# Kernel tuning notes

Hardware: AMD Instinct MI355X
Metric: run time of the kernel (lower is better)

Reference implementation:

```python
import jax, jax.numpy as jnp
import numpy as np

N_POINTS = 100000
N_EVENTS = 1000000
N_PAIRS = 100000      # node_pair_samples
N_RIEMANN = 128       # riemann_samples
INIT_BETA = 0.025
NON_EVENT_W = 1.0
EPS = 1e-6            # torch PairwiseDistance default eps (added to the difference)


def setup_inputs() -> dict:
    key = jax.random.key(0)
    ks = jax.random.split(key, 8)
    # learned parameters
    beta = jnp.full((1, 1), INIT_BETA, jnp.float32)
    z0 = jax.random.uniform(ks[0], (N_POINTS, 2), jnp.float32, -0.025, 0.025)
    v0 = jax.random.uniform(ks[1], (N_POINTS, 2), jnp.float32, -0.025, 0.025)
    a0 = jnp.zeros((N_POINTS, 2), jnp.float32)  # a0 is referenced by step(); zero -> constant-velocity
    # event data: (u, v, event_time)
    u = jax.random.randint(ks[2], (N_EVENTS,), 0, N_POINTS)
    v = jax.random.randint(ks[3], (N_EVENTS,), 0, N_POINTS)
    event_times = jax.random.uniform(ks[4], (N_EVENTS,), jnp.float32, 0.0, 1.0)
    # sampled non-event node pairs (stand-in for randperm over triu indices)
    pair_u = jax.random.randint(ks[5], (N_PAIRS,), 0, N_POINTS)
    pair_v = jax.random.randint(ks[6], (N_PAIRS,), 0, N_POINTS)
    pair_v = jnp.where(pair_v == pair_u, (pair_v + 1) % N_POINTS, pair_v)
    t0 = jnp.float32(0.0)
    tn = jnp.float32(1.0)
    return {"beta": beta, "z0": z0, "v0": v0, "a0": a0,
            "u": u, "v": v, "event_times": event_times,
            "pair_u": pair_u, "pair_v": pair_v, "t0": t0, "tn": tn}


def reference(beta, z0, v0, a0, u, v, event_times, pair_u, pair_v, t0, tn):
    b = beta[0, 0]
    # ---- event intensity: sum_e (beta - ||z_u(t_e) - z_v(t_e)||) ----
    te = event_times[:, None]                                  # [E,1]
    zu = z0[u] + v0[u] * te + 0.5 * a0[u] * te ** 2            # [E,2]
    zv = z0[v] + v0[v] * te + 0.5 * a0[v] * te ** 2            # [E,2]
    d_ev = jnp.sqrt(jnp.sum((zu - zv + EPS) ** 2, axis=-1))    # [E]
    event_intensity = b * event_times.shape[0] - jnp.sum(d_ev)
    # ---- non-event intensity: Riemann sum of exp(beta - d(t)) over sampled pairs ----
    ts = t0 + (jnp.arange(N_RIEMANN, dtype=jnp.float32) / N_RIEMANN) * (tn - t0)  # [T] left Riemann
    dt = (tn - t0) / N_RIEMANN
    dz = z0[pair_u] - z0[pair_v]                               # [P,2]
    dv = v0[pair_u] - v0[pair_v]
    da = a0[pair_u] - a0[pair_v]
    tt = ts[None, :, None]                                     # [1,T,1]
    diff = dz[:, None, :] + dv[:, None, :] * tt + 0.5 * da[:, None, :] * tt ** 2 + EPS  # [P,T,2]
    d_ne = jnp.sqrt(jnp.sum(diff ** 2, axis=-1))               # [P,T]
    non_event_intensity = jnp.sum(jnp.exp(b - d_ne)) * dt
    return event_intensity - NON_EVENT_W * non_event_intensity
```

## Files before the change

### kernel.cpp

```cpp
#include <hip/hip_runtime.h>
#include <hip/hip_fp16.h>

#define N_POINTS   100000
#define N_EVENTS   1000000
#define N_PAIRS    100000
#define N_RIEMANN  128
#define EPS_F      1e-6f
#define NON_EVENT_W 1.0f

constexpr int BLOCK       = 256;

constexpr int EVPT        = 8;
constexpr int EV_THREADS  = N_EVENTS / EVPT;
constexpr int EV_BLOCKS   = (EV_THREADS + BLOCK - 1) / BLOCK;

constexpr int RPT          = 32;
constexpr int CHUNKS       = N_RIEMANN / RPT;
constexpr int PAIR_THREADS = N_PAIRS * CHUNKS;
constexpr int PAIR_BLOCKS  = (PAIR_THREADS + BLOCK - 1) / BLOCK;

constexpr int MAIN_BLOCKS = PAIR_BLOCKS + EV_BLOCKS;
constexpr int PREP_BLOCKS = (N_POINTS + BLOCK - 1) / BLOCK;


__device__ __forceinline__ float block_reduce_sum(float v) {
    #pragma unroll
    for (int off = 32; off > 0; off >>= 1)
        v += __shfl_down(v, off, 64);
    __shared__ float smem[BLOCK / 64];
    const int lane = threadIdx.x & 63;
    const int wid  = threadIdx.x >> 6;
    if (lane == 0) smem[wid] = v;
    __syncthreads();
    float r = 0.f;
    if (threadIdx.x == 0) {
        #pragma unroll
        for (int i = 0; i < BLOCK / 64; ++i) r += smem[i];
    }
    return r;
}

__device__ __forceinline__ void decode_rec(const float4& r, float2& z, float2& v, float2& a) {
    z = __half22float2(*reinterpret_cast<const __half2*>(&r.x));
    v = __half22float2(*reinterpret_cast<const __half2*>(&r.y));
    a = __half22float2(*reinterpret_cast<const __half2*>(&r.z));
}

__global__ __launch_bounds__(BLOCK) void prep_kernel(
    const float2* __restrict__ z0,
    const float2* __restrict__ v0,
    const float2* __restrict__ a0,
    float4*       __restrict__ pts)
{
    const int i = blockIdx.x * BLOCK + threadIdx.x;
    if (i < N_POINTS) {
        const float2 z = z0[i], v = v0[i], a = a0[i];
        float4 r;
        *reinterpret_cast<__half2*>(&r.x) = __float22half2_rn(make_float2(z.x, z.y));
        *reinterpret_cast<__half2*>(&r.y) = __float22half2_rn(make_float2(v.x, v.y));
        *reinterpret_cast<__half2*>(&r.z) = __float22half2_rn(make_float2(a.x, a.y));
        r.w = 0.f;
        pts[i] = r;
    }
}

template <bool PACKED>
__global__ __launch_bounds__(BLOCK) void main_kernel(
    const float4* __restrict__ pts,
    const float2* __restrict__ z0,
    const float2* __restrict__ v0,
    const float2* __restrict__ a0,
    const float*  __restrict__ beta,
    const int*    __restrict__ eu,
    const int*    __restrict__ ev,
    const float*  __restrict__ et,
    const int*    __restrict__ pu,
    const int*    __restrict__ pv,
    const float*  __restrict__ t0p,
    const float*  __restrict__ tnp,
    float*        __restrict__ partials)
{
    float acc = 0.f;
    const int b = blockIdx.x;

    if (b < PAIR_BLOCKS) {
        const int p = b * BLOCK + threadIdx.x;
        if (p < PAIR_THREADS) {
            const int chunk = p / N_PAIRS;
            const int pr    = p - chunk * N_PAIRS;
            const float t0v = t0p[0];
            const float tnv = tnp[0];
            const float step = (tnv - t0v) * (1.0f / N_RIEMANN);
            const float bb  = beta[0];
            const int iu = pu[pr];
            const int iv = pv[pr];
            float dzx, dzy, dvx, dvy, dax, day;
            if (PACKED) {
                const float4 ru = pts[iu];
                const float4 rv = pts[iv];
                float2 zu, vu, au, zv, vv, av;
                decode_rec(ru, zu, vu, au);
                decode_rec(rv, zv, vv, av);
                dzx = zu.x - zv.x; dzy = zu.y - zv.y;
                dvx = vu.x - vv.x; dvy = vu.y - vv.y;
                dax = au.x - av.x; day = au.y - av.y;
            } else {
                const float2 zu = z0[iu], zv = z0[iv];
                const float2 vu = v0[iu], vv = v0[iv];
                const float2 au = a0[iu], av = a0[iv];
                dzx = zu.x - zv.x; dzy = zu.y - zv.y;
                dvx = vu.x - vv.x; dvy = vu.y - vv.y;
                dax = au.x - av.x; day = au.y - av.y;
            }
            const float dzxe = dzx + EPS_F;
            const float dzye = dzy + EPS_F;
            const float hax  = 0.5f * dax;
            const float hay  = 0.5f * day;
            const float eb = __expf(bb);
            float s = 0.f;
            const int k0 = chunk * RPT;
            #pragma unroll 8
            for (int k = k0; k < k0 + RPT; ++k) {
                const float t  = __fmaf_rn((float)k, step, t0v);
                const float h  = t * t;
                const float dx = __fmaf_rn(hax, h, __fmaf_rn(dvx, t, dzxe));
                const float dy = __fmaf_rn(hay, h, __fmaf_rn(dvy, t, dzye));
                const float d  = __builtin_amdgcn_sqrtf(__fmaf_rn(dy, dy, dx * dx));
                s += __expf(-d);
            }
            acc = -NON_EVENT_W * step * eb * s;
        }
    } else {
        const int t = (b - PAIR_BLOCKS) * BLOCK + threadIdx.x;
        if (t < EV_THREADS) {
            const int4*   eu4 = reinterpret_cast<const int4*>(eu);
            const int4*   ev4 = reinterpret_cast<const int4*>(ev);
            const float4* et4 = reinterpret_cast<const float4*>(et);
            const int4 u0 = eu4[2 * t], u1 = eu4[2 * t + 1];
            const int4 w0 = ev4[2 * t], w1 = ev4[2 * t + 1];
            const float4 t0q = et4[2 * t], t1q = et4[2 * t + 1];
            const int iu[EVPT] = { u0.x, u0.y, u0.z, u0.w, u1.x, u1.y, u1.z, u1.w };
            const int iv[EVPT] = { w0.x, w0.y, w0.z, w0.w, w1.x, w1.y, w1.z, w1.w };
            const float te[EVPT] = { t0q.x, t0q.y, t0q.z, t0q.w, t1q.x, t1q.y, t1q.z, t1q.w };
            if (PACKED) {
                float4 ru[EVPT], rv[EVPT];
                #pragma unroll
                for (int j = 0; j < EVPT; ++j) ru[j] = pts[iu[j]];
                #pragma unroll
                for (int j = 0; j < EVPT; ++j) rv[j] = pts[iv[j]];
                #pragma unroll
                for (int j = 0; j < EVPT; ++j) {
                    float2 zu, vu, au, zv, vv, av;
                    decode_rec(ru[j], zu, vu, au);
                    decode_rec(rv[j], zv, vv, av);
                    const float h = 0.5f * te[j] * te[j];
                    const float dx = (zu.x - zv.x) + (vu.x - vv.x) * te[j] + (au.x - av.x) * h + EPS_F;
                    const float dy = (zu.y - zv.y) + (vu.y - vv.y) * te[j] + (au.y - av.y) * h + EPS_F;
                    acc -= __builtin_amdgcn_sqrtf(__fmaf_rn(dy, dy, dx * dx));
                }
            } else {
                #pragma unroll
                for (int j = 0; j < EVPT; ++j) {
                    const float2 zu = z0[iu[j]], zv = z0[iv[j]];
                    const float2 vu = v0[iu[j]], vv = v0[iv[j]];
                    const float2 au = a0[iu[j]], av = a0[iv[j]];
                    const float h = 0.5f * te[j] * te[j];
                    const float dx = (zu.x - zv.x) + (vu.x - vv.x) * te[j] + (au.x - av.x) * h + EPS_F;
                    const float dy = (zu.y - zv.y) + (vu.y - vv.y) * te[j] + (au.y - av.y) * h + EPS_F;
                    acc -= __builtin_amdgcn_sqrtf(__fmaf_rn(dy, dy, dx * dx));
                }
            }
        }
    }

    const float r = block_reduce_sum(acc);
    if (threadIdx.x == 0) partials[blockIdx.x] = r;
}

__global__ __launch_bounds__(BLOCK) void reduce_kernel(
    const float* __restrict__ partials,
    const float* __restrict__ beta,
    float*       __restrict__ out)
{
    float acc = 0.f;
    for (int i = threadIdx.x; i < MAIN_BLOCKS; i += BLOCK) acc += partials[i];
    const float r = block_reduce_sum(acc);
    if (threadIdx.x == 0) out[0] = beta[0] * (float)N_EVENTS + r;
}

extern "C" void kernel_launch(void* const* d_in, const int* in_sizes, int n_in,
                              void* d_out, int out_size, void* d_ws, size_t ws_size,
                              hipStream_t stream) {
    const float*  beta = (const float*)d_in[0];
    const float2* z0   = (const float2*)d_in[1];
    const float2* v0   = (const float2*)d_in[2];
    const float2* a0   = (const float2*)d_in[3];
    const int*    eu   = (const int*)d_in[4];
    const int*    ev   = (const int*)d_in[5];
    const float*  et   = (const float*)d_in[6];
    const int*    pu   = (const int*)d_in[7];
    const int*    pv   = (const int*)d_in[8];
    const float*  t0p  = (const float*)d_in[9];
    const float*  tnp  = (const float*)d_in[10];

    float* out = (float*)d_out;
    const size_t pts_bytes = (size_t)N_POINTS * sizeof(float4);
    const bool packed = (ws_size >= pts_bytes + (size_t)MAIN_BLOCKS * sizeof(float));

    if (packed) {
        float4* pts      = (float4*)d_ws;
        float*  partials = (float*)((char*)d_ws + pts_bytes);
        prep_kernel<<<PREP_BLOCKS, BLOCK, 0, stream>>>(z0, v0, a0, pts);
        main_kernel<true><<<MAIN_BLOCKS, BLOCK, 0, stream>>>(
            pts, z0, v0, a0, beta, eu, ev, et, pu, pv, t0p, tnp, partials);
        reduce_kernel<<<1, BLOCK, 0, stream>>>(partials, beta, out);
    } else {
        float* partials = (float*)d_ws;
        main_kernel<false><<<MAIN_BLOCKS, BLOCK, 0, stream>>>(
            nullptr, z0, v0, a0, beta, eu, ev, et, pu, pv, t0p, tnp, partials);
        reduce_kernel<<<1, BLOCK, 0, stream>>>(partials, beta, out);
    }
}
```

Measured before the change: 101.8 us.

## Fuse prep, main and reduce kernels into one cooperative persistent kernel

Replaces the three launches (fp16 packing, main compute, final reduce) with a single cooperative kernel that uses grid-wide syncs between phases. A persistent grid sized from occupancy for 256 CUs loops over the virtual blocks, with event blocks now ordered before pair blocks. This removes launch gaps and two kernel boundaries, but adds grid-sync overhead and cooperative-launch constraints. Block 0 does the final reduction after the second grid sync.

```diff
diff --git a/kernel.cpp b/kernel.cpp
--- a/kernel.cpp
+++ b/kernel.cpp
@@ -1,5 +1,8 @@
 #include <hip/hip_runtime.h>
 #include <hip/hip_fp16.h>
+#include <hip/hip_cooperative_groups.h>
+
+namespace cg = cooperative_groups;
 
 #define N_POINTS   100000
 #define N_EVENTS   1000000
@@ -8,19 +11,18 @@
 #define EPS_F      1e-6f
 #define NON_EVENT_W 1.0f
 
-constexpr int BLOCK       = 256;
-
-constexpr int EVPT        = 8;
-constexpr int EV_THREADS  = N_EVENTS / EVPT;
-constexpr int EV_BLOCKS   = (EV_THREADS + BLOCK - 1) / BLOCK;
+constexpr int BLOCK = 256;
+
+constexpr int EVPT       = 8;
+constexpr int EV_THREADS = N_EVENTS / EVPT;
+constexpr int EV_BLOCKS  = (EV_THREADS + BLOCK - 1) / BLOCK;
 
 constexpr int RPT          = 32;
 constexpr int CHUNKS       = N_RIEMANN / RPT;
 constexpr int PAIR_THREADS = N_PAIRS * CHUNKS;
 constexpr int PAIR_BLOCKS  = (PAIR_THREADS + BLOCK - 1) / BLOCK;
 
-constexpr int MAIN_BLOCKS = PAIR_BLOCKS + EV_BLOCKS;
-constexpr int PREP_BLOCKS = (N_POINTS + BLOCK - 1) / BLOCK;
+constexpr int VB_TOTAL = EV_BLOCKS + PAIR_BLOCKS;
 
 
 __device__ __forceinline__ float block_reduce_sum(float v) {
@@ -46,27 +48,9 @@
     a = __half22float2(*reinterpret_cast<const __half2*>(&r.z));
 }
 
-__global__ __launch_bounds__(BLOCK) void prep_kernel(
-    const float2* __restrict__ z0,
-    const float2* __restrict__ v0,
-    const float2* __restrict__ a0,
-    float4*       __restrict__ pts)
-{
-    const int i = blockIdx.x * BLOCK + threadIdx.x;
-    if (i < N_POINTS) {
-        const float2 z = z0[i], v = v0[i], a = a0[i];
-        float4 r;
-        *reinterpret_cast<__half2*>(&r.x) = __float22half2_rn(make_float2(z.x, z.y));
-        *reinterpret_cast<__half2*>(&r.y) = __float22half2_rn(make_float2(v.x, v.y));
-        *reinterpret_cast<__half2*>(&r.z) = __float22half2_rn(make_float2(a.x, a.y));
-        r.w = 0.f;
-        pts[i] = r;
-    }
-}
-
 template <bool PACKED>
-__global__ __launch_bounds__(BLOCK) void main_kernel(
-    const float4* __restrict__ pts,
+__global__ __launch_bounds__(BLOCK) void fused_kernel(
+    float4*       __restrict__ pts,
     const float2* __restrict__ z0,
     const float2* __restrict__ v0,
     const float2* __restrict__ a0,
@@ -78,114 +62,129 @@
     const int*    __restrict__ pv,
     const float*  __restrict__ t0p,
     const float*  __restrict__ tnp,
-    float*        __restrict__ partials)
+    float*        __restrict__ partials,
+    float*        __restrict__ out)
 {
+    const int G = gridDim.x;
+
+    if constexpr (PACKED) {
+        for (int i = blockIdx.x * BLOCK + threadIdx.x; i < N_POINTS; i += G * BLOCK) {
+            const float2 z = z0[i], v = v0[i], a = a0[i];
+            float4 r;
+            *reinterpret_cast<__half2*>(&r.x) = __float22half2_rn(make_float2(z.x, z.y));
+            *reinterpret_cast<__half2*>(&r.y) = __float22half2_rn(make_float2(v.x, v.y));
+            *reinterpret_cast<__half2*>(&r.z) = __float22half2_rn(make_float2(a.x, a.y));
+            r.w = 0.f;
+            pts[i] = r;
+        }
+        cg::this_grid().sync();
+    }
+
+    const float t0v  = t0p[0];
+    const float tnv  = tnp[0];
+    const float bb   = beta[0];
+    const float step = (tnv - t0v) * (1.0f / N_RIEMANN);
+    const float neg_dt_eb = -NON_EVENT_W * step * __expf(bb);
+
     float acc = 0.f;
-    const int b = blockIdx.x;
-
-    if (b < PAIR_BLOCKS) {
-        const int p = b * BLOCK + threadIdx.x;
-        if (p < PAIR_THREADS) {
-            const int chunk = p / N_PAIRS;
-            const int pr    = p - chunk * N_PAIRS;
-            const float t0v = t0p[0];
-            const float tnv = tnp[0];
-            const float step = (tnv - t0v) * (1.0f / N_RIEMANN);
-            const float bb  = beta[0];
-            const int iu = pu[pr];
-            const int iv = pv[pr];
-            float dzx, dzy, dvx, dvy, dax, day;
-            if (PACKED) {
-                const float4 ru = pts[iu];
-                const float4 rv = pts[iv];
-                float2 zu, vu, au, zv, vv, av;
-                decode_rec(ru, zu, vu, au);
-                decode_rec(rv, zv, vv, av);
-                dzx = zu.x - zv.x; dzy = zu.y - zv.y;
-                dvx = vu.x - vv.x; dvy = vu.y - vv.y;
-                dax = au.x - av.x; day = au.y - av.y;
-            } else {
-                const float2 zu = z0[iu], zv = z0[iv];
-                const float2 vu = v0[iu], vv = v0[iv];
-                const float2 au = a0[iu], av = a0[iv];
-                dzx = zu.x - zv.x; dzy = zu.y - zv.y;
-                dvx = vu.x - vv.x; dvy = vu.y - vv.y;
-                dax = au.x - av.x; day = au.y - av.y;
-            }
-            const float dzxe = dzx + EPS_F;
-            const float dzye = dzy + EPS_F;
-            const float hax  = 0.5f * dax;
-            const float hay  = 0.5f * day;
-            const float eb = __expf(bb);
-            float s = 0.f;
-            const int k0 = chunk * RPT;
-            #pragma unroll 8
-            for (int k = k0; k < k0 + RPT; ++k) {
-                const float t  = __fmaf_rn((float)k, step, t0v);
-                const float h  = t * t;
-                const float dx = __fmaf_rn(hax, h, __fmaf_rn(dvx, t, dzxe));
-                const float dy = __fmaf_rn(hay, h, __fmaf_rn(dvy, t, dzye));
-                const float d  = __builtin_amdgcn_sqrtf(__fmaf_rn(dy, dy, dx * dx));
-                s += __expf(-d);
-            }
-            acc = -NON_EVENT_W * step * eb * s;
-        }
-    } else {
-        const int t = (b - PAIR_BLOCKS) * BLOCK + threadIdx.x;
-        if (t < EV_THREADS) {
-            const int4*   eu4 = reinterpret_cast<const int4*>(eu);
-            const int4*   ev4 = reinterpret_cast<const int4*>(ev);
-            const float4* et4 = reinterpret_cast<const float4*>(et);
-            const int4 u0 = eu4[2 * t], u1 = eu4[2 * t + 1];
-            const int4 w0 = ev4[2 * t], w1 = ev4[2 * t + 1];
-            const float4 t0q = et4[2 * t], t1q = et4[2 * t + 1];
-            const int iu[EVPT] = { u0.x, u0.y, u0.z, u0.w, u1.x, u1.y, u1.z, u1.w };
-            const int iv[EVPT] = { w0.x, w0.y, w0.z, w0.w, w1.x, w1.y, w1.z, w1.w };
-            const float te[EVPT] = { t0q.x, t0q.y, t0q.z, t0q.w, t1q.x, t1q.y, t1q.z, t1q.w };
-            if (PACKED) {
-                float4 ru[EVPT], rv[EVPT];
-                #pragma unroll
-                for (int j = 0; j < EVPT; ++j) ru[j] = pts[iu[j]];
-                #pragma unroll
-                for (int j = 0; j < EVPT; ++j) rv[j] = pts[iv[j]];
-                #pragma unroll
-                for (int j = 0; j < EVPT; ++j) {
-                    float2 zu, vu, au, zv, vv, av;
-                    decode_rec(ru[j], zu, vu, au);
-                    decode_rec(rv[j], zv, vv, av);
-                    const float h = 0.5f * te[j] * te[j];
-                    const float dx = (zu.x - zv.x) + (vu.x - vv.x) * te[j] + (au.x - av.x) * h + EPS_F;
-                    const float dy = (zu.y - zv.y) + (vu.y - vv.y) * te[j] + (au.y - av.y) * h + EPS_F;
-                    acc -= __builtin_amdgcn_sqrtf(__fmaf_rn(dy, dy, dx * dx));
-                }
-            } else {
-                #pragma unroll
-                for (int j = 0; j < EVPT; ++j) {
-                    const float2 zu = z0[iu[j]], zv = z0[iv[j]];
-                    const float2 vu = v0[iu[j]], vv = v0[iv[j]];
-                    const float2 au = a0[iu[j]], av = a0[iv[j]];
-                    const float h = 0.5f * te[j] * te[j];
-                    const float dx = (zu.x - zv.x) + (vu.x - vv.x) * te[j] + (au.x - av.x) * h + EPS_F;
-                    const float dy = (zu.y - zv.y) + (vu.y - vv.y) * te[j] + (au.y - av.y) * h + EPS_F;
-                    acc -= __builtin_amdgcn_sqrtf(__fmaf_rn(dy, dy, dx * dx));
+
+    for (int vb = blockIdx.x; vb < VB_TOTAL; vb += G) {
+        if (vb < EV_BLOCKS) {
+            const int t = vb * BLOCK + threadIdx.x;
+            if (t < EV_THREADS) {
+                const int4*   eu4 = reinterpret_cast<const int4*>(eu);
+                const int4*   ev4 = reinterpret_cast<const int4*>(ev);
+                const float4* et4 = reinterpret_cast<const float4*>(et);
+                const int4 u0 = eu4[2 * t], u1 = eu4[2 * t + 1];
+                const int4 w0 = ev4[2 * t], w1 = ev4[2 * t + 1];
+                const float4 t0q = et4[2 * t], t1q = et4[2 * t + 1];
+                const int iu[EVPT] = { u0.x, u0.y, u0.z, u0.w, u1.x, u1.y, u1.z, u1.w };
+                const int iv[EVPT] = { w0.x, w0.y, w0.z, w0.w, w1.x, w1.y, w1.z, w1.w };
+                const float te[EVPT] = { t0q.x, t0q.y, t0q.z, t0q.w, t1q.x, t1q.y, t1q.z, t1q.w };
+                if constexpr (PACKED) {
+                    float4 ru[EVPT], rv[EVPT];
+                    #pragma unroll
+                    for (int j = 0; j < EVPT; ++j) ru[j] = pts[iu[j]];
+                    #pragma unroll
+                    for (int j = 0; j < EVPT; ++j) rv[j] = pts[iv[j]];
+                    #pragma unroll
+                    for (int j = 0; j < EVPT; ++j) {
+                        float2 zu, vu, au, zv, vv, av;
+                        decode_rec(ru[j], zu, vu, au);
+                        decode_rec(rv[j], zv, vv, av);
+                        const float h = 0.5f * te[j] * te[j];
+                        const float dx = (zu.x - zv.x) + (vu.x - vv.x) * te[j] + (au.x - av.x) * h + EPS_F;
+                        const float dy = (zu.y - zv.y) + (vu.y - vv.y) * te[j] + (au.y - av.y) * h + EPS_F;
+                        acc -= __builtin_amdgcn_sqrtf(__fmaf_rn(dy, dy, dx * dx));
+                    }
+                } else {
+                    #pragma unroll
+                    for (int j = 0; j < EVPT; ++j) {
+                        const float2 zu = z0[iu[j]], zv = z0[iv[j]];
+                        const float2 vu = v0[iu[j]], vv = v0[iv[j]];
+                        const float2 au = a0[iu[j]], av = a0[iv[j]];
+                        const float h = 0.5f * te[j] * te[j];
+                        const float dx = (zu.x - zv.x) + (vu.x - vv.x) * te[j] + (au.x - av.x) * h + EPS_F;
+                        const float dy = (zu.y - zv.y) + (vu.y - vv.y) * te[j] + (au.y - av.y) * h + EPS_F;
+                        acc -= __builtin_amdgcn_sqrtf(__fmaf_rn(dy, dy, dx * dx));
+                    }
                 }
             }
+        } else {
+            const int p = (vb - EV_BLOCKS) * BLOCK + threadIdx.x;
+            if (p < PAIR_THREADS) {
+                const int chunk = p / N_PAIRS;
+                const int pr    = p - chunk * N_PAIRS;
+                const int iu = pu[pr];
+                const int iv = pv[pr];
+                float dzx, dzy, dvx, dvy, dax, day;
+                if constexpr (PACKED) {
+                    const float4 ru = pts[iu];
+                    const float4 rv = pts[iv];
+                    float2 zu, vu, au, zv, vv, av;
+                    decode_rec(ru, zu, vu, au);
+                    decode_rec(rv, zv, vv, av);
+                    dzx = zu.x - zv.x; dzy = zu.y - zv.y;
+                    dvx = vu.x - vv.x; dvy = vu.y - vv.y;
+                    dax = au.x - av.x; day = au.y - av.y;
+                } else {
+                    const float2 zu = z0[iu], zv = z0[iv];
+                    const float2 vu = v0[iu], vv = v0[iv];
+                    const float2 au = a0[iu], av = a0[iv];
+                    dzx = zu.x - zv.x; dzy = zu.y - zv.y;
+                    dvx = vu.x - vv.x; dvy = vu.y - vv.y;
+                    dax = au.x - av.x; day = au.y - av.y;
+                }
+                const float dzxe = dzx + EPS_F;
+                const float dzye = dzy + EPS_F;
+                const float hax  = 0.5f * dax;
+                const float hay  = 0.5f * day;
+                float s = 0.f;
+                const int k0 = chunk * RPT;
+                #pragma unroll 8
+                for (int k = k0; k < k0 + RPT; ++k) {
+                    const float t  = __fmaf_rn((float)k, step, t0v);
+                    const float h  = t * t;
+                    const float dx = __fmaf_rn(hax, h, __fmaf_rn(dvx, t, dzxe));
+                    const float dy = __fmaf_rn(hay, h, __fmaf_rn(dvy, t, dzye));
+                    const float d  = __builtin_amdgcn_sqrtf(__fmaf_rn(dy, dy, dx * dx));
+                    s += __expf(-d);
+                }
+                acc += neg_dt_eb * s;
+            }
         }
     }
 
     const float r = block_reduce_sum(acc);
     if (threadIdx.x == 0) partials[blockIdx.x] = r;
-}
-
-__global__ __launch_bounds__(BLOCK) void reduce_kernel(
-    const float* __restrict__ partials,
-    const float* __restrict__ beta,
-    float*       __restrict__ out)
-{
-    float acc = 0.f;
-    for (int i = threadIdx.x; i < MAIN_BLOCKS; i += BLOCK) acc += partials[i];
-    const float r = block_reduce_sum(acc);
-    if (threadIdx.x == 0) out[0] = beta[0] * (float)N_EVENTS + r;
+    cg::this_grid().sync();
+
+    if (blockIdx.x == 0) {
+        float a2 = 0.f;
+        for (int i = threadIdx.x; i < G; i += BLOCK) a2 += partials[i];
+        const float rr = block_reduce_sum(a2);
+        if (threadIdx.x == 0) out[0] = bb * (float)N_EVENTS + rr;
+    }
 }
 
 extern "C" void kernel_launch(void* const* d_in, const int* in_sizes, int n_in,
@@ -205,19 +204,29 @@
 
     float* out = (float*)d_out;
     const size_t pts_bytes = (size_t)N_POINTS * sizeof(float4);
-    const bool packed = (ws_size >= pts_bytes + (size_t)MAIN_BLOCKS * sizeof(float));
+
+    static int grid_packed = 0, grid_plain = 0;
+    if (grid_packed == 0) {
+        int nb = 0;
+        if (hipOccupancyMaxActiveBlocksPerMultiprocessor(&nb, fused_kernel<true>, BLOCK, 0) != hipSuccess || nb < 1) nb = 2;
+        grid_packed = nb * 256;
+        if (grid_packed > VB_TOTAL) grid_packed = VB_TOTAL;
+        nb = 0;
+        if (hipOccupancyMaxActiveBlocksPerMultiprocessor(&nb, fused_kernel<false>, BLOCK, 0) != hipSuccess || nb < 1) nb = 2;
+        grid_plain = nb * 256;
+        if (grid_plain > VB_TOTAL) grid_plain = VB_TOTAL;
+    }
+
+    const bool packed = (ws_size >= pts_bytes + (size_t)VB_TOTAL * sizeof(float));
+    float4* pts      = packed ? (float4*)d_ws : nullptr;
+    float*  partials = packed ? (float*)((char*)d_ws + pts_bytes) : (float*)d_ws;
+
+    void* args[] = { &pts, &z0, &v0, &a0, &beta, &eu, &ev, &et,
+                     &pu, &pv, &t0p, &tnp, &partials, &out };
 
     if (packed) {
-        float4* pts      = (float4*)d_ws;
-        float*  partials = (float*)((char*)d_ws + pts_bytes);
-        prep_kernel<<<PREP_BLOCKS, BLOCK, 0, stream>>>(z0, v0, a0, pts);
-        main_kernel<true><<<MAIN_BLOCKS, BLOCK, 0, stream>>>(
-            pts, z0, v0, a0, beta, eu, ev, et, pu, pv, t0p, tnp, partials);
-        reduce_kernel<<<1, BLOCK, 0, stream>>>(partials, beta, out);
+        hipLaunchCooperativeKernel(fused_kernel<true>,  dim3(grid_packed), dim3(BLOCK), args, 0, stream);
     } else {
-        float* partials = (float*)d_ws;
-        main_kernel<false><<<MAIN_BLOCKS, BLOCK, 0, stream>>>(
-            nullptr, z0, v0, a0, beta, eu, ev, et, pu, pv, t0p, tnp, partials);
-        reduce_kernel<<<1, BLOCK, 0, stream>>>(partials, beta, out);
-    }
-}
+        hipLaunchCooperativeKernel(fused_kernel<false>, dim3(grid_plain),  dim3(BLOCK), args, 0, stream);
+    }
+}
```

Result: slower. 262.6 us (+157.9%).

## Interleave event and pair blocks and cut events per thread to two

Applied to the files above, without the earlier changes.

Events per thread drop from 8 to 2, which gives four times as many event blocks with fewer gathers in flight per thread. Block indices are remapped by proportional interleaving, so event blocks and pair-Riemann blocks spread evenly across the grid instead of running as two phases. This is meant to mix memory-bound gather work with compute-bound exp/sqrt work on each CU and to raise occupancy. The cost is more blocks, more partial sums to reduce, and less memory-level parallelism per thread.

```diff
diff --git a/kernel.cpp b/kernel.cpp
--- a/kernel.cpp
+++ b/kernel.cpp
@@ -8,18 +8,19 @@
 #define EPS_F      1e-6f
 #define NON_EVENT_W 1.0f
 
-constexpr int BLOCK       = 256;
-
-constexpr int EVPT        = 8;
-constexpr int EV_THREADS  = N_EVENTS / EVPT;
-constexpr int EV_BLOCKS   = (EV_THREADS + BLOCK - 1) / BLOCK;
+constexpr int BLOCK = 256;
+
+constexpr int EVPT       = 2;
+constexpr int EV_THREADS = N_EVENTS / EVPT;
+constexpr int EV_BLOCKS  = (EV_THREADS + BLOCK - 1) / BLOCK;
 
 constexpr int RPT          = 32;
 constexpr int CHUNKS       = N_RIEMANN / RPT;
 constexpr int PAIR_THREADS = N_PAIRS * CHUNKS;
 constexpr int PAIR_BLOCKS  = (PAIR_THREADS + BLOCK - 1) / BLOCK;
 
-constexpr int MAIN_BLOCKS = PAIR_BLOCKS + EV_BLOCKS;
+constexpr int VB_TOTAL = EV_BLOCKS + PAIR_BLOCKS;
+
 constexpr int PREP_BLOCKS = (N_POINTS + BLOCK - 1) / BLOCK;
 
 
@@ -83,19 +84,70 @@
     float acc = 0.f;
     const int b = blockIdx.x;
 
-    if (b < PAIR_BLOCKS) {
-        const int p = b * BLOCK + threadIdx.x;
+    const int f0 = (int)(((long long)b       * EV_BLOCKS) / VB_TOTAL);
+    const int f1 = (int)(((long long)(b + 1) * EV_BLOCKS) / VB_TOTAL);
+
+    if (f1 > f0) {
+        const int t = f0 * BLOCK + threadIdx.x;
+        if (t < EV_THREADS) {
+            const int2*   eu2 = reinterpret_cast<const int2*>(eu);
+            const int2*   ev2 = reinterpret_cast<const int2*>(ev);
+            const float2* et2 = reinterpret_cast<const float2*>(et);
+            const int2   u  = eu2[t];
+            const int2   w  = ev2[t];
+            const float2 tq = et2[t];
+            if constexpr (PACKED) {
+                const float4 ru0 = pts[u.x];
+                const float4 rv0 = pts[w.x];
+                const float4 ru1 = pts[u.y];
+                const float4 rv1 = pts[w.y];
+                {
+                    float2 zu, vu, au, zv, vv, av;
+                    decode_rec(ru0, zu, vu, au);
+                    decode_rec(rv0, zv, vv, av);
+                    const float h  = 0.5f * tq.x * tq.x;
+                    const float dx = (zu.x - zv.x) + (vu.x - vv.x) * tq.x + (au.x - av.x) * h + EPS_F;
+                    const float dy = (zu.y - zv.y) + (vu.y - vv.y) * tq.x + (au.y - av.y) * h + EPS_F;
+                    acc -= __builtin_amdgcn_sqrtf(__fmaf_rn(dy, dy, dx * dx));
+                }
+                {
+                    float2 zu, vu, au, zv, vv, av;
+                    decode_rec(ru1, zu, vu, au);
+                    decode_rec(rv1, zv, vv, av);
+                    const float h  = 0.5f * tq.y * tq.y;
+                    const float dx = (zu.x - zv.x) + (vu.x - vv.x) * tq.y + (au.x - av.x) * h + EPS_F;
+                    const float dy = (zu.y - zv.y) + (vu.y - vv.y) * tq.y + (au.y - av.y) * h + EPS_F;
+                    acc -= __builtin_amdgcn_sqrtf(__fmaf_rn(dy, dy, dx * dx));
+                }
+            } else {
+                #pragma unroll
+                for (int j = 0; j < EVPT; ++j) {
+                    const int   iu = (j == 0) ? u.x : u.y;
+                    const int   iv = (j == 0) ? w.x : w.y;
+                    const float te = (j == 0) ? tq.x : tq.y;
+                    const float2 zu = z0[iu], zv = z0[iv];
+                    const float2 vu = v0[iu], vv = v0[iv];
+                    const float2 au = a0[iu], av = a0[iv];
+                    const float h  = 0.5f * te * te;
+                    const float dx = (zu.x - zv.x) + (vu.x - vv.x) * te + (au.x - av.x) * h + EPS_F;
+                    const float dy = (zu.y - zv.y) + (vu.y - vv.y) * te + (au.y - av.y) * h + EPS_F;
+                    acc -= __builtin_amdgcn_sqrtf(__fmaf_rn(dy, dy, dx * dx));
+                }
+            }
+        }
+    } else {
+        const int p = (b - f0) * BLOCK + threadIdx.x;
         if (p < PAIR_THREADS) {
             const int chunk = p / N_PAIRS;
             const int pr    = p - chunk * N_PAIRS;
-            const float t0v = t0p[0];
-            const float tnv = tnp[0];
+            const float t0v  = t0p[0];
+            const float tnv  = tnp[0];
             const float step = (tnv - t0v) * (1.0f / N_RIEMANN);
-            const float bb  = beta[0];
+            const float bb   = beta[0];
             const int iu = pu[pr];
             const int iv = pv[pr];
             float dzx, dzy, dvx, dvy, dax, day;
-            if (PACKED) {
+            if constexpr (PACKED) {
                 const float4 ru = pts[iu];
                 const float4 rv = pts[iv];
                 float2 zu, vu, au, zv, vv, av;
@@ -116,7 +168,6 @@
             const float dzye = dzy + EPS_F;
             const float hax  = 0.5f * dax;
             const float hay  = 0.5f * day;
-            const float eb = __expf(bb);
             float s = 0.f;
             const int k0 = chunk * RPT;
             #pragma unroll 8
@@ -128,48 +179,7 @@
                 const float d  = __builtin_amdgcn_sqrtf(__fmaf_rn(dy, dy, dx * dx));
                 s += __expf(-d);
             }
-            acc = -NON_EVENT_W * step * eb * s;
-        }
-    } else {
-        const int t = (b - PAIR_BLOCKS) * BLOCK + threadIdx.x;
-        if (t < EV_THREADS) {
-            const int4*   eu4 = reinterpret_cast<const int4*>(eu);
-            const int4*   ev4 = reinterpret_cast<const int4*>(ev);
-            const float4* et4 = reinterpret_cast<const float4*>(et);
-            const int4 u0 = eu4[2 * t], u1 = eu4[2 * t + 1];
-            const int4 w0 = ev4[2 * t], w1 = ev4[2 * t + 1];
-            const float4 t0q = et4[2 * t], t1q = et4[2 * t + 1];
-            const int iu[EVPT] = { u0.x, u0.y, u0.z, u0.w, u1.x, u1.y, u1.z, u1.w };
-            const int iv[EVPT] = { w0.x, w0.y, w0.z, w0.w, w1.x, w1.y, w1.z, w1.w };
-            const float te[EVPT] = { t0q.x, t0q.y, t0q.z, t0q.w, t1q.x, t1q.y, t1q.z, t1q.w };
-            if (PACKED) {
-                float4 ru[EVPT], rv[EVPT];
-                #pragma unroll
-                for (int j = 0; j < EVPT; ++j) ru[j] = pts[iu[j]];
-                #pragma unroll
-                for (int j = 0; j < EVPT; ++j) rv[j] = pts[iv[j]];
-                #pragma unroll
-                for (int j = 0; j < EVPT; ++j) {
-                    float2 zu, vu, au, zv, vv, av;
-                    decode_rec(ru[j], zu, vu, au);
-                    decode_rec(rv[j], zv, vv, av);
-                    const float h = 0.5f * te[j] * te[j];
-                    const float dx = (zu.x - zv.x) + (vu.x - vv.x) * te[j] + (au.x - av.x) * h + EPS_F;
-                    const float dy = (zu.y - zv.y) + (vu.y - vv.y) * te[j] + (au.y - av.y) * h + EPS_F;
-                    acc -= __builtin_amdgcn_sqrtf(__fmaf_rn(dy, dy, dx * dx));
-                }
-            } else {
-                #pragma unroll
-                for (int j = 0; j < EVPT; ++j) {
-                    const float2 zu = z0[iu[j]], zv = z0[iv[j]];
-                    const float2 vu = v0[iu[j]], vv = v0[iv[j]];
-                    const float2 au = a0[iu[j]], av = a0[iv[j]];
-                    const float h = 0.5f * te[j] * te[j];
-                    const float dx = (zu.x - zv.x) + (vu.x - vv.x) * te[j] + (au.x - av.x) * h + EPS_F;
-                    const float dy = (zu.y - zv.y) + (vu.y - vv.y) * te[j] + (au.y - av.y) * h + EPS_F;
-                    acc -= __builtin_amdgcn_sqrtf(__fmaf_rn(dy, dy, dx * dx));
-                }
-            }
+            acc = -NON_EVENT_W * step * __expf(bb) * s;
         }
     }
 
@@ -183,7 +193,7 @@
     float*       __restrict__ out)
 {
     float acc = 0.f;
-    for (int i = threadIdx.x; i < MAIN_BLOCKS; i += BLOCK) acc += partials[i];
+    for (int i = threadIdx.x; i < VB_TOTAL; i += BLOCK) acc += partials[i];
     const float r = block_reduce_sum(acc);
     if (threadIdx.x == 0) out[0] = beta[0] * (float)N_EVENTS + r;
 }
@@ -205,18 +215,18 @@
 
     float* out = (float*)d_out;
     const size_t pts_bytes = (size_t)N_POINTS * sizeof(float4);
-    const bool packed = (ws_size >= pts_bytes + (size_t)MAIN_BLOCKS * sizeof(float));
+    const bool packed = (ws_size >= pts_bytes + (size_t)VB_TOTAL * sizeof(float));
 
     if (packed) {
         float4* pts      = (float4*)d_ws;
         float*  partials = (float*)((char*)d_ws + pts_bytes);
         prep_kernel<<<PREP_BLOCKS, BLOCK, 0, stream>>>(z0, v0, a0, pts);
-        main_kernel<true><<<MAIN_BLOCKS, BLOCK, 0, stream>>>(
+        main_kernel<true><<<VB_TOTAL, BLOCK, 0, stream>>>(
             pts, z0, v0, a0, beta, eu, ev, et, pu, pv, t0p, tnp, partials);
         reduce_kernel<<<1, BLOCK, 0, stream>>>(partials, beta, out);
     } else {
         float* partials = (float*)d_ws;
-        main_kernel<false><<<MAIN_BLOCKS, BLOCK, 0, stream>>>(
+        main_kernel<false><<<VB_TOTAL, BLOCK, 0, stream>>>(
             nullptr, z0, v0, a0, beta, eu, ev, et, pu, pv, t0p, tnp, partials);
         reduce_kernel<<<1, BLOCK, 0, stream>>>(partials, beta, out);
     }
```

New measurement: 104.2 us. +2.3%, slower.
